# Optimization experiments

Hardware: AMD Instinct MI355X
Metric: run time of the kernel (lower is better)

## Reference

```python
import jax, jax.numpy as jnp
import numpy as np

H = 16   # heads
D = 64   # dim_heads
E = 1024 # embed_dim


def setup_inputs() -> dict:
    key = jax.random.key(0)
    ks = jax.random.split(key, 13)
    B, T = 4, 2048
    s_in = 1.0 / np.sqrt(E)
    s_out = 1.0 / np.sqrt(H * D)
    return {
        "q": jax.random.normal(ks[0], (B, T, E), jnp.float32),
        "k": jax.random.normal(ks[1], (B, T, E), jnp.float32),
        "v": jax.random.normal(ks[2], (B, T, E), jnp.float32),
        "Wq": jax.random.normal(ks[3], (E, H * D), jnp.float32) * s_in,
        "bq": jax.random.normal(ks[4], (H * D,), jnp.float32) * s_in,
        "Wk": jax.random.normal(ks[5], (E, H * D), jnp.float32) * s_in,
        "bk": jax.random.normal(ks[6], (H * D,), jnp.float32) * s_in,
        "Wv": jax.random.normal(ks[7], (E, H * D), jnp.float32) * s_in,
        "bv": jax.random.normal(ks[8], (H * D,), jnp.float32) * s_in,
        "Wo": jax.random.normal(ks[9], (H * D, E), jnp.float32) * s_out,
        "bo": jax.random.normal(ks[10], (E,), jnp.float32) * s_out,
    }


def reference(q, k, v, Wq, bq, Wk, bk, Wv, bv, Wo, bo):
    B, T, _ = q.shape
    scale = jnp.sqrt(jnp.asarray(E, q.dtype))  # note: sqrt(embed_dim), as in source
    # NOTE: source does .view(B, H, T, D) on contiguous (B, T, H*D) -> raw reshape.
    qh = (q @ Wq + bq).reshape(B, H, T, D)
    kh = (k @ Wk + bk).reshape(B, H, T, D)
    vh = (v @ Wv + bv).reshape(B, H, T, D)
    attn = jnp.einsum("bhtd,bhsd->bhts", qh, kh) / scale  # (B,H,T,T)
    causal = jnp.tril(jnp.ones((T, T), dtype=bool))
    attn = jnp.where(causal, attn, -jnp.inf)
    p = jax.nn.softmax(attn, axis=-1)
    out = jnp.einsum("bhts,bhsd->bhtd", p, vh)  # (B,H,T,D)
    out = out.transpose(0, 2, 1, 3).reshape(B, T, H * D)
    return out @ Wo + bo
```

## Files before the change

### kernel.cpp

```cpp
#include <hip/hip_runtime.h>
#include <hip/hip_bf16.h>
#include <math.h>


typedef unsigned short ushort_t;
typedef __attribute__((ext_vector_type(8))) short s8v;
typedef __attribute__((ext_vector_type(8))) unsigned short us8;
typedef __attribute__((ext_vector_type(4))) float f4v;

#define BAR()    __builtin_amdgcn_s_barrier()
#define LFENCE() asm volatile("" ::: "memory")
#define VMCNT(n) asm volatile("s_waitcnt vmcnt(" #n ")" ::: "memory")

__device__ __forceinline__ unsigned short f2bf(float x) {
  __hip_bfloat16 h = __float2bfloat16(x);
  unsigned short u; __builtin_memcpy(&u, &h, 2); return u;
}

__device__ __forceinline__ void gload16(const void* g, void* l) {
  __builtin_amdgcn_global_load_lds(
      (const __attribute__((address_space(1))) unsigned int*)g,
      (__attribute__((address_space(3))) unsigned int*)l, 16, 0, 0);
}

__global__ __launch_bounds__(256) void castk3(const float* __restrict__ q,
                                              const float* __restrict__ k,
                                              const float* __restrict__ v,
                                              ushort_t* __restrict__ dst) {
  const int y = blockIdx.y;
  const float* src = (y == 0) ? q : (y == 1) ? k : v;
  ushort_t* d = dst + (size_t)y * 8388608;
  int i = blockIdx.x * 256 + threadIdx.x;
  const float4* s4 = (const float4*)src + (size_t)i * 2;
  float4 a = s4[0], b = s4[1];
  us8 o;
  o[0]=f2bf(a.x); o[1]=f2bf(a.y); o[2]=f2bf(a.z); o[3]=f2bf(a.w);
  o[4]=f2bf(b.x); o[5]=f2bf(b.y); o[6]=f2bf(b.z); o[7]=f2bf(b.w);
  *(us8*)(d + (size_t)i * 8) = o;
}

__global__ __launch_bounds__(256) void wtrans4(
    const float* __restrict__ W0, const float* __restrict__ W1,
    const float* __restrict__ W2, const float* __restrict__ W3,
    ushort_t* __restrict__ Wt) {
  __shared__ unsigned tr[64][65];
  const int z = blockIdx.z;
  const float* W = (z == 0) ? W0 : (z == 1) ? W1 : (z == 2) ? W2 : W3;
  ushort_t* dst = Wt + (size_t)z * 1048576;
  const int k0 = blockIdx.y * 64, n0 = blockIdx.x * 64;
  const int tid = threadIdx.x;
  {
    const int rr = tid >> 4, c4 = tid & 15;
#pragma unroll
    for (int p = 0; p < 4; ++p) {
      const int k = p * 16 + rr;
      float4 v = *(const float4*)(W + (size_t)(k0 + k) * 1024 + n0 + c4 * 4);
      tr[c4*4+0][k] = f2bf(v.x); tr[c4*4+1][k] = f2bf(v.y);
      tr[c4*4+2][k] = f2bf(v.z); tr[c4*4+3][k] = f2bf(v.w);
    }
  }
  __syncthreads();
  const int r = tid >> 3, s = tid & 7;
#pragma unroll
  for (int p = 0; p < 2; ++p) {
    const int n = p * 32 + r;
    us8 o;
#pragma unroll
    for (int j = 0; j < 8; ++j) o[j] = (ushort_t)tr[n][s*8+j];
    *(us8*)(dst + (size_t)(n0 + n) * 1024 + k0 + s * 8) = o;
  }
}

__global__ __launch_bounds__(256) void vtrans(const ushort_t* __restrict__ Pv,
                                              ushort_t* __restrict__ Pvt) {
  __shared__ unsigned tr[64][65];
  const int t0 = blockIdx.x * 64, hd = blockIdx.y;
  const ushort_t* src = Pv + (size_t)hd * 131072;
  ushort_t* dst = Pvt + (size_t)hd * 131072;
  const int tid = threadIdx.x;
  const int r = tid >> 3, s = tid & 7;
#pragma unroll
  for (int p = 0; p < 2; ++p) {
    const int t = p * 32 + r;
    us8 v = *(const us8*)(src + (size_t)(t0 + t) * 64 + s * 8);
#pragma unroll
    for (int j = 0; j < 8; ++j) tr[s*8+j][t] = v[j];
  }
  __syncthreads();
#pragma unroll
  for (int p = 0; p < 2; ++p) {
    const int d = p * 32 + r;
    us8 o;
#pragma unroll
    for (int j = 0; j < 8; ++j) o[j] = (ushort_t)tr[d][s*8+j];
    *(us8*)(dst + (size_t)d * 2048 + t0 + s * 8) = o;
  }
}

template<int OUTF32>
__global__ __launch_bounds__(256) void gemm_bf16(
    const ushort_t* __restrict__ A, const ushort_t* __restrict__ Bt,
    const float* __restrict__ bias, void* __restrict__ Cout,
    int Mdim, int Ndim, int Kdim)
{
  __shared__ __align__(16) ushort_t As[2][128 * 64];
  __shared__ __align__(16) ushort_t Bs[2][128 * 64];
  const int tid = threadIdx.x;
  const int m0 = blockIdx.y * 128, n0 = blockIdx.x * 128;
  const int w = tid >> 6, lane = tid & 63, lo = lane & 15, hi = lane >> 4;
  const int wm = (w >> 1) * 64, wn = (w & 1) * 64;
  const int srow = tid >> 3, sslot = tid & 7;

  f4v acc[4][4];
#pragma unroll
  for (int i = 0; i < 4; ++i)
#pragma unroll
    for (int j = 0; j < 4; ++j) { f4v z = {0.f,0.f,0.f,0.f}; acc[i][j] = z; }

  const int NT = Kdim >> 6;

#define G_STAGE(buf, k0)                                                     \
  {                                                                          \
    _Pragma("unroll")                                                        \
    for (int i = 0; i < 4; ++i) {                                            \
      const int row = i * 32 + srow;                                         \
      const int sw = (sslot ^ (row & 7)) * 8;                                \
      gload16(A  + (size_t)(m0 + row) * Kdim + (k0) + sw,                    \
              &As[buf][(i * 256 + tid) * 8]);                                \
      gload16(Bt + (size_t)(n0 + row) * Kdim + (k0) + sw,                    \
              &Bs[buf][(i * 256 + tid) * 8]);                                \
    }                                                                        \
  }

  G_STAGE(0, 0);
  int cur = 0;
  for (int t = 0; t < NT; ++t) {
    if (t + 1 < NT) { G_STAGE(cur ^ 1, (t + 1) * 64); VMCNT(8); }
    else            { VMCNT(0); }
    BAR(); LFENCE();
    const ushort_t* Ab = &As[cur][0];
    const ushort_t* Bb = &Bs[cur][0];
#pragma unroll
    for (int ks = 0; ks < 2; ++ks) {
      const int slot = ks * 4 + hi;
      s8v av[4], bv[4];
#pragma unroll
      for (int i = 0; i < 4; ++i) {
        const int ra = wm + i * 16 + lo;
        av[i] = *(const s8v*)&Ab[ra * 64 + ((slot ^ (ra & 7)) << 3)];
        const int rb = wn + i * 16 + lo;
        bv[i] = *(const s8v*)&Bb[rb * 64 + ((slot ^ (rb & 7)) << 3)];
      }
#pragma unroll
      for (int am = 0; am < 4; ++am)
#pragma unroll
        for (int an = 0; an < 4; ++an)
          acc[am][an] = __builtin_amdgcn_mfma_f32_16x16x32_bf16(
              av[am], bv[an], acc[am][an], 0, 0, 0);
    }
    LFENCE(); BAR();
    cur ^= 1;
  }
#undef G_STAGE

#pragma unroll
  for (int an = 0; an < 4; ++an) {
    const int n = n0 + wn + an * 16 + lo;
    const float bsv = bias[n];
#pragma unroll
    for (int am = 0; am < 4; ++am) {
      const int mb = m0 + wm + am * 16 + hi * 4;
#pragma unroll
      for (int r = 0; r < 4; ++r) {
        const float v = acc[am][an][r] + bsv;
        if (OUTF32) ((float*)Cout)[(size_t)(mb + r) * Ndim + n] = v;
        else ((ushort_t*)Cout)[(size_t)(mb + r) * Ndim + n] = f2bf(v);
      }
    }
  }
}

__global__ __launch_bounds__(256) void attn_mfma(
    const ushort_t* __restrict__ Pq, const ushort_t* __restrict__ Pk,
    const ushort_t* __restrict__ Pvt, ushort_t* __restrict__ Ao)
{
  __shared__ __align__(16) ushort_t Ks[2][64 * 64];
  __shared__ __align__(16) ushort_t Vts[2][64 * 64];
  __shared__ __align__(16) ushort_t Psb[64 * 64];

  const int tid = threadIdx.x;
  const int id = blockIdx.x;
  const int qt = 31 - (id >> 6);
  const int hd = id & 63;
  const int b = hd >> 4, h = hd & 15;
  const int w = tid >> 6, lane = tid & 63, lo = lane & 15, hi = lane >> 4;
  const ushort_t* Qh = Pq + (size_t)hd * 131072;
  const ushort_t* Kh = Pk + (size_t)hd * 131072;
  const ushort_t* Vh = Pvt + (size_t)hd * 131072;
  const int srow = tid >> 3, sslot = tid & 7;

  s8v qa[2];
#pragma unroll
  for (int ks = 0; ks < 2; ++ks)
    qa[ks] = *(const s8v*)(Qh + (size_t)(qt * 64 + w * 16 + lo) * 64 + ks * 32 + hi * 8);

  f4v od[4];
#pragma unroll
  for (int f = 0; f < 4; ++f) { f4v z = {0.f,0.f,0.f,0.f}; od[f] = z; }
  float m[4], l[4];
#pragma unroll
  for (int r = 0; r < 4; ++r) { m[r] = -INFINITY; l[r] = 0.f; }

#define A_STAGE(buf, kt_)                                                    \
  {                                                                          \
    _Pragma("unroll")                                                        \
    for (int i = 0; i < 2; ++i) {                                            \
      const int row = i * 32 + srow;                                         \
      const int sw = (sslot ^ (row & 7)) * 8;                                \
      gload16(Kh + (size_t)((kt_) * 64 + row) * 64 + sw,                     \
              &Ks[buf][(i * 256 + tid) * 8]);                                \
      gload16(Vh + (size_t)row * 2048 + (kt_) * 64 + sw,                     \
              &Vts[buf][(i * 256 + tid) * 8]);                               \
    }                                                                        \
  }

  A_STAGE(0, 0);
  int cur = 0;
  for (int kt = 0; kt <= qt; ++kt) {
    if (kt < qt) { A_STAGE(cur ^ 1, kt + 1); VMCNT(4); }
    else         { VMCNT(0); }
    BAR(); LFENCE();
    const ushort_t* Kb = &Ks[cur][0];
    const ushort_t* Vb = &Vts[cur][0];

    f4v sf[4];
#pragma unroll
    for (int f = 0; f < 4; ++f) { f4v z = {0.f,0.f,0.f,0.f}; sf[f] = z; }
    __builtin_amdgcn_s_setprio(1);
#pragma unroll
    for (int ks = 0; ks < 2; ++ks) {
      const int slot = ks * 4 + hi;
      s8v kb[4];
#pragma unroll
      for (int f = 0; f < 4; ++f) {
        const int rk = f * 16 + lo;
        kb[f] = *(const s8v*)&Kb[rk * 64 + ((slot ^ (rk & 7)) << 3)];
      }
#pragma unroll
      for (int f = 0; f < 4; ++f)
        sf[f] = __builtin_amdgcn_mfma_f32_16x16x32_bf16(qa[ks], kb[f], sf[f], 0, 0, 0);
    }
    __builtin_amdgcn_s_setprio(0);

    float sc[4][4];
#pragma unroll
    for (int f = 0; f < 4; ++f)
#pragma unroll
      for (int r = 0; r < 4; ++r) sc[r][f] = sf[f][r] * 0.03125f;
    if (kt == qt) {
#pragma unroll
      for (int r = 0; r < 4; ++r)
#pragma unroll
        for (int f = 0; f < 4; ++f)
          if (16 * f + lo > 16 * w + 4 * hi + r) sc[r][f] = -INFINITY;
    }
    float rmax[4];
#pragma unroll
    for (int r = 0; r < 4; ++r)
      rmax[r] = fmaxf(fmaxf(sc[r][0], sc[r][1]), fmaxf(sc[r][2], sc[r][3]));
#pragma unroll
    for (int x = 1; x < 16; x <<= 1)
#pragma unroll
      for (int r = 0; r < 4; ++r) rmax[r] = fmaxf(rmax[r], __shfl_xor(rmax[r], x, 64));
#pragma unroll
    for (int r = 0; r < 4; ++r) {
      const float mn = fmaxf(m[r], rmax[r]);
      const float al = __expf(m[r] - mn);
      m[r] = mn;
      float rs = 0.f;
#pragma unroll
      for (int f = 0; f < 4; ++f) {
        const float p = __expf(sc[r][f] - mn);
        sc[r][f] = p; rs += p;
      }
      l[r] = l[r] * al + rs;
#pragma unroll
      for (int f = 0; f < 4; ++f) od[f][r] *= al;
    }

#pragma unroll
    for (int r = 0; r < 4; ++r) {
      const int t = 16 * w + 4 * hi + r;
#pragma unroll
      for (int f = 0; f < 4; ++f) {
        const int s = 16 * f + lo;
        Psb[t * 64 + (((s >> 3) ^ (t & 7)) << 3) + (s & 7)] = f2bf(sc[r][f]);
      }
    }

    {
      const int t = 16 * w + lo;
      __builtin_amdgcn_s_setprio(1);
#pragma unroll
      for (int ks = 0; ks < 2; ++ks) {
        const int slot = ks * 4 + hi;
        s8v pa = *(const s8v*)&Psb[t * 64 + ((slot ^ (t & 7)) << 3)];
        s8v vb[4];
#pragma unroll
        for (int f = 0; f < 4; ++f) {
          const int rd = f * 16 + lo;
          vb[f] = *(const s8v*)&Vb[rd * 64 + ((slot ^ (rd & 7)) << 3)];
        }
#pragma unroll
        for (int f = 0; f < 4; ++f)
          od[f] = __builtin_amdgcn_mfma_f32_16x16x32_bf16(pa, vb[f], od[f], 0, 0, 0);
      }
      __builtin_amdgcn_s_setprio(0);
    }
    LFENCE(); BAR();
    cur ^= 1;
  }
#undef A_STAGE

#pragma unroll
  for (int x = 1; x < 16; x <<= 1)
#pragma unroll
    for (int r = 0; r < 4; ++r) l[r] += __shfl_xor(l[r], x, 64);
  float inv[4];
#pragma unroll
  for (int r = 0; r < 4; ++r) inv[r] = 1.0f / l[r];
#pragma unroll
  for (int f = 0; f < 4; ++f)
#pragma unroll
    for (int r = 0; r < 4; ++r) {
      const int t = qt * 64 + 16 * w + 4 * hi + r;
      const int d = 16 * f + lo;
      Ao[(size_t)(b * 2048 + t) * 1024 + h * 64 + d] = f2bf(od[f][r] * inv[r]);
    }
}

extern "C" void kernel_launch(void* const* d_in, const int* in_sizes, int n_in,
                              void* d_out, int out_size, void* d_ws, size_t ws_size,
                              hipStream_t stream) {
  const float* q  = (const float*)d_in[0];
  const float* k  = (const float*)d_in[1];
  const float* v  = (const float*)d_in[2];
  const float* Wq = (const float*)d_in[3];
  const float* bq = (const float*)d_in[4];
  const float* Wk = (const float*)d_in[5];
  const float* bk = (const float*)d_in[6];
  const float* Wv = (const float*)d_in[7];
  const float* bv = (const float*)d_in[8];
  const float* Wo = (const float*)d_in[9];
  const float* bo = (const float*)d_in[10];
  float* out = (float*)d_out;

  char* wsb = (char*)d_ws;
  ushort_t* qb  = (ushort_t*)(wsb + 0);
  ushort_t* kb  = (ushort_t*)(wsb + 16777216);
  ushort_t* Wqt = (ushort_t*)(wsb + 50331648);
  ushort_t* Pq  = (ushort_t*)(wsb + 58720256);
  ushort_t* Pk  = (ushort_t*)(wsb + 75497472);
  ushort_t* Pv  = (ushort_t*)(wsb + 92274688);
  ushort_t* Wkt = Wqt + 1048576;
  ushort_t* Wvt = Wqt + 2097152;
  ushort_t* Wot = Wqt + 3145728;
  ushort_t* vb  = (ushort_t*)(wsb + 33554432);
  ushort_t* Pvt = qb;
  ushort_t* Ao  = kb;

  castk3<<<dim3(4096, 3), 256, 0, stream>>>(q, k, v, qb);
  wtrans4<<<dim3(16, 16, 4), 256, 0, stream>>>(Wq, Wk, Wv, Wo, Wqt);

  gemm_bf16<0><<<dim3(8, 64), 256, 0, stream>>>(qb, Wqt, bq, Pq, 8192, 1024, 1024);
  gemm_bf16<0><<<dim3(8, 64), 256, 0, stream>>>(kb, Wkt, bk, Pk, 8192, 1024, 1024);
  gemm_bf16<0><<<dim3(8, 64), 256, 0, stream>>>(vb, Wvt, bv, Pv, 8192, 1024, 1024);

  vtrans<<<dim3(32, 64), 256, 0, stream>>>(Pv, Pvt);
  attn_mfma<<<2048, 256, 0, stream>>>(Pq, Pk, Pvt, Ao);

  gemm_bf16<1><<<dim3(8, 64), 256, 0, stream>>>(Ao, Wot, bo, out, 8192, 1024, 1024);
}
```

Measured before the change: 367.9 us.

## Batch QKV GEMMs, enlarge attention tiles, fold scale into Q, use exp2 with lazy rescale

Merges the three projection GEMMs into one launch with a z-dimension and bakes log2e/sqrt(E) into the Q projection output. The attention kernel now uses 512 threads covering 128 query rows per block, and uses exp2 instead of exp. It skips the cross-lane max reduction and rescale when no row max grows by more than a threshold. The K loop is unrolled by two with fixed buffers, and the GEMM dimensions are hardcoded. This cuts launch count, repeated K/V loads and softmax overhead, at the cost of extra masking work on the diagonal and a larger block.

```diff
diff --git a/kernel.cpp b/kernel.cpp
--- a/kernel.cpp
+++ b/kernel.cpp
@@ -15,6 +15,10 @@
 __device__ __forceinline__ unsigned short f2bf(float x) {
   __hip_bfloat16 h = __float2bfloat16(x);
   unsigned short u; __builtin_memcpy(&u, &h, 2); return u;
+}
+
+__device__ __forceinline__ float exp2a(float x) {
+  return __builtin_amdgcn_exp2f(x);
 }
 
 __device__ __forceinline__ void gload16(const void* g, void* l) {
@@ -98,15 +102,13 @@
 }
 
 template<int OUTF32>
-__global__ __launch_bounds__(256) void gemm_bf16(
+__device__ __forceinline__ void gemm_body(
+    ushort_t* As, ushort_t* Bs,
     const ushort_t* __restrict__ A, const ushort_t* __restrict__ Bt,
     const float* __restrict__ bias, void* __restrict__ Cout,
-    int Mdim, int Ndim, int Kdim)
+    float scale, int m0, int n0)
 {
-  __shared__ __align__(16) ushort_t As[2][128 * 64];
-  __shared__ __align__(16) ushort_t Bs[2][128 * 64];
   const int tid = threadIdx.x;
-  const int m0 = blockIdx.y * 128, n0 = blockIdx.x * 128;
   const int w = tid >> 6, lane = tid & 63, lo = lane & 15, hi = lane >> 4;
   const int wm = (w >> 1) * 64, wn = (w & 1) * 64;
   const int srow = tid >> 3, sslot = tid & 7;
@@ -117,29 +119,19 @@
 #pragma unroll
     for (int j = 0; j < 4; ++j) { f4v z = {0.f,0.f,0.f,0.f}; acc[i][j] = z; }
 
-  const int NT = Kdim >> 6;
-
-#define G_STAGE(buf, k0)                                                     \
-  {                                                                          \
-    _Pragma("unroll")                                                        \
-    for (int i = 0; i < 4; ++i) {                                            \
-      const int row = i * 32 + srow;                                         \
-      const int sw = (sslot ^ (row & 7)) * 8;                                \
-      gload16(A  + (size_t)(m0 + row) * Kdim + (k0) + sw,                    \
-              &As[buf][(i * 256 + tid) * 8]);                                \
-      gload16(Bt + (size_t)(n0 + row) * Kdim + (k0) + sw,                    \
-              &Bs[buf][(i * 256 + tid) * 8]);                                \
-    }                                                                        \
-  }
-
-  G_STAGE(0, 0);
-  int cur = 0;
-  for (int t = 0; t < NT; ++t) {
-    if (t + 1 < NT) { G_STAGE(cur ^ 1, (t + 1) * 64); VMCNT(8); }
-    else            { VMCNT(0); }
-    BAR(); LFENCE();
-    const ushort_t* Ab = &As[cur][0];
-    const ushort_t* Bb = &Bs[cur][0];
+  auto stage = [&](int buf, int kt) {
+    ushort_t* Ad = &As[buf * 8192];
+    ushort_t* Bd = &Bs[buf * 8192];
+#pragma unroll
+    for (int i = 0; i < 4; ++i) {
+      const int row = i * 32 + srow;
+      const int sw = (sslot ^ (row & 7)) * 8;
+      gload16(A  + (size_t)(m0 + row) * 1024 + kt * 64 + sw, &Ad[(i * 256 + tid) * 8]);
+      gload16(Bt + (size_t)(n0 + row) * 1024 + kt * 64 + sw, &Bd[(i * 256 + tid) * 8]);
+    }
+  };
+
+  auto compute = [&](const ushort_t* Ab, const ushort_t* Bb) {
 #pragma unroll
     for (int ks = 0; ks < 2; ++ks) {
       const int slot = ks * 4 + hi;
@@ -158,10 +150,20 @@
           acc[am][an] = __builtin_amdgcn_mfma_f32_16x16x32_bf16(
               av[am], bv[an], acc[am][an], 0, 0, 0);
     }
+  };
+
+  stage(0, 0);
+  for (int t = 0; t < 16; t += 2) {
+    stage(1, t + 1); VMCNT(8);
+    BAR(); LFENCE();
+    compute(&As[0], &Bs[0]);
     LFENCE(); BAR();
-    cur ^= 1;
-  }
-#undef G_STAGE
+    if (t + 2 < 16) { stage(0, t + 2); VMCNT(8); }
+    else            { VMCNT(0); }
+    BAR(); LFENCE();
+    compute(&As[8192], &Bs[8192]);
+    LFENCE(); BAR();
+  }
 
 #pragma unroll
   for (int an = 0; an < 4; ++an) {
@@ -172,25 +174,51 @@
       const int mb = m0 + wm + am * 16 + hi * 4;
 #pragma unroll
       for (int r = 0; r < 4; ++r) {
-        const float v = acc[am][an][r] + bsv;
-        if (OUTF32) ((float*)Cout)[(size_t)(mb + r) * Ndim + n] = v;
-        else ((ushort_t*)Cout)[(size_t)(mb + r) * Ndim + n] = f2bf(v);
-      }
-    }
-  }
-}
-
-__global__ __launch_bounds__(256) void attn_mfma(
+        const float v = (acc[am][an][r] + bsv) * scale;
+        if (OUTF32) ((float*)Cout)[(size_t)(mb + r) * 1024 + n] = v;
+        else ((ushort_t*)Cout)[(size_t)(mb + r) * 1024 + n] = f2bf(v);
+      }
+    }
+  }
+}
+
+__global__ __launch_bounds__(256) void gemm_qkv(
+    const ushort_t* __restrict__ Abase, const ushort_t* __restrict__ Wbase,
+    const float* __restrict__ bq, const float* __restrict__ bk,
+    const float* __restrict__ bv, ushort_t* __restrict__ Cbase)
+{
+  __shared__ __align__(16) ushort_t As[2 * 8192];
+  __shared__ __align__(16) ushort_t Bs[2 * 8192];
+  const int z = blockIdx.z;
+  const ushort_t* A  = Abase + (size_t)z * 8388608;
+  const ushort_t* Bt = Wbase + (size_t)z * 1048576;
+  const float* bias = (z == 0) ? bq : (z == 1) ? bk : bv;
+  const float scale = (z == 0) ? 0.04508422002778011f : 1.0f;
+  gemm_body<0>(As, Bs, A, Bt, bias, Cbase + (size_t)z * 8388608,
+               scale, blockIdx.y * 128, blockIdx.x * 128);
+}
+
+__global__ __launch_bounds__(256) void gemm_out(
+    const ushort_t* __restrict__ A, const ushort_t* __restrict__ Bt,
+    const float* __restrict__ bias, float* __restrict__ Cout)
+{
+  __shared__ __align__(16) ushort_t As[2 * 8192];
+  __shared__ __align__(16) ushort_t Bs[2 * 8192];
+  gemm_body<1>(As, Bs, A, Bt, bias, Cout, 1.0f,
+               blockIdx.y * 128, blockIdx.x * 128);
+}
+
+__global__ __launch_bounds__(512) void attn_mfma(
     const ushort_t* __restrict__ Pq, const ushort_t* __restrict__ Pk,
     const ushort_t* __restrict__ Pvt, ushort_t* __restrict__ Ao)
 {
-  __shared__ __align__(16) ushort_t Ks[2][64 * 64];
-  __shared__ __align__(16) ushort_t Vts[2][64 * 64];
-  __shared__ __align__(16) ushort_t Psb[64 * 64];
+  __shared__ __align__(16) ushort_t Ks[2 * 4096];
+  __shared__ __align__(16) ushort_t Vts[2 * 4096];
+  __shared__ __align__(16) ushort_t Psb[128 * 64];
 
   const int tid = threadIdx.x;
   const int id = blockIdx.x;
-  const int qt = 31 - (id >> 6);
+  const int qt = 15 - (id >> 6);
   const int hd = id & 63;
   const int b = hd >> 4, h = hd & 15;
   const int w = tid >> 6, lane = tid & 63, lo = lane & 15, hi = lane >> 4;
@@ -198,41 +226,31 @@
   const ushort_t* Kh = Pk + (size_t)hd * 131072;
   const ushort_t* Vh = Pvt + (size_t)hd * 131072;
   const int srow = tid >> 3, sslot = tid & 7;
+  const int qt2 = 2 * qt;
 
   s8v qa[2];
 #pragma unroll
   for (int ks = 0; ks < 2; ++ks)
-    qa[ks] = *(const s8v*)(Qh + (size_t)(qt * 64 + w * 16 + lo) * 64 + ks * 32 + hi * 8);
+    qa[ks] = *(const s8v*)(Qh + (size_t)(qt * 128 + w * 16 + lo) * 64 + ks * 32 + hi * 8);
 
   f4v od[4];
 #pragma unroll
   for (int f = 0; f < 4; ++f) { f4v z = {0.f,0.f,0.f,0.f}; od[f] = z; }
   float m[4], l[4];
-#pragma unroll
-  for (int r = 0; r < 4; ++r) { m[r] = -INFINITY; l[r] = 0.f; }
-
-#define A_STAGE(buf, kt_)                                                    \
-  {                                                                          \
-    _Pragma("unroll")                                                        \
-    for (int i = 0; i < 2; ++i) {                                            \
-      const int row = i * 32 + srow;                                         \
-      const int sw = (sslot ^ (row & 7)) * 8;                                \
-      gload16(Kh + (size_t)((kt_) * 64 + row) * 64 + sw,                     \
-              &Ks[buf][(i * 256 + tid) * 8]);                                \
-      gload16(Vh + (size_t)row * 2048 + (kt_) * 64 + sw,                     \
-              &Vts[buf][(i * 256 + tid) * 8]);                               \
-    }                                                                        \
-  }
-
-  A_STAGE(0, 0);
-  int cur = 0;
-  for (int kt = 0; kt <= qt; ++kt) {
-    if (kt < qt) { A_STAGE(cur ^ 1, kt + 1); VMCNT(4); }
-    else         { VMCNT(0); }
-    BAR(); LFENCE();
-    const ushort_t* Kb = &Ks[cur][0];
-    const ushort_t* Vb = &Vts[cur][0];
-
+  int tg[4];
+#pragma unroll
+  for (int r = 0; r < 4; ++r) {
+    m[r] = -INFINITY; l[r] = 0.f;
+    tg[r] = qt * 128 + 16 * w + 4 * hi + r;
+  }
+
+  auto astage = [&](int buf, int kt) {
+    const int sw = (sslot ^ (srow & 7)) * 8;
+    gload16(Kh + (size_t)(kt * 64 + srow) * 64 + sw, &Ks[buf * 4096 + tid * 8]);
+    gload16(Vh + (size_t)srow * 2048 + kt * 64 + sw, &Vts[buf * 4096 + tid * 8]);
+  };
+
+  auto acompute = [&](const ushort_t* Kb, const ushort_t* Vb, int kt_) {
     f4v sf[4];
 #pragma unroll
     for (int f = 0; f < 4; ++f) { f4v z = {0.f,0.f,0.f,0.f}; sf[f] = z; }
@@ -256,36 +274,48 @@
 #pragma unroll
     for (int f = 0; f < 4; ++f)
 #pragma unroll
-      for (int r = 0; r < 4; ++r) sc[r][f] = sf[f][r] * 0.03125f;
-    if (kt == qt) {
+      for (int r = 0; r < 4; ++r) sc[r][f] = sf[f][r];
+    if (kt_ >= qt2) {
 #pragma unroll
       for (int r = 0; r < 4; ++r)
 #pragma unroll
         for (int f = 0; f < 4; ++f)
-          if (16 * f + lo > 16 * w + 4 * hi + r) sc[r][f] = -INFINITY;
-    }
-    float rmax[4];
+          if (kt_ * 64 + 16 * f + lo > tg[r]) sc[r][f] = -INFINITY;
+    }
+
+    float lmax[4];
 #pragma unroll
     for (int r = 0; r < 4; ++r)
-      rmax[r] = fmaxf(fmaxf(sc[r][0], sc[r][1]), fmaxf(sc[r][2], sc[r][3]));
-#pragma unroll
-    for (int x = 1; x < 16; x <<= 1)
-#pragma unroll
-      for (int r = 0; r < 4; ++r) rmax[r] = fmaxf(rmax[r], __shfl_xor(rmax[r], x, 64));
+      lmax[r] = fmaxf(fmaxf(sc[r][0], sc[r][1]), fmaxf(sc[r][2], sc[r][3]));
+    const int ok = (lmax[0] <= m[0] + 8.f) & (lmax[1] <= m[1] + 8.f) &
+                   (lmax[2] <= m[2] + 8.f) & (lmax[3] <= m[3] + 8.f);
+    if (!__all(ok)) {
+      float rmax[4];
+#pragma unroll
+      for (int r = 0; r < 4; ++r) rmax[r] = lmax[r];
+#pragma unroll
+      for (int x = 1; x < 16; x <<= 1)
+#pragma unroll
+        for (int r = 0; r < 4; ++r)
+          rmax[r] = fmaxf(rmax[r], __shfl_xor(rmax[r], x, 64));
+#pragma unroll
+      for (int r = 0; r < 4; ++r) {
+        const float mn = fmaxf(m[r], rmax[r]);
+        const float al = exp2a(m[r] - mn);
+        m[r] = mn; l[r] *= al;
+#pragma unroll
+        for (int f = 0; f < 4; ++f) od[f][r] *= al;
+      }
+    }
 #pragma unroll
     for (int r = 0; r < 4; ++r) {
-      const float mn = fmaxf(m[r], rmax[r]);
-      const float al = __expf(m[r] - mn);
-      m[r] = mn;
       float rs = 0.f;
 #pragma unroll
       for (int f = 0; f < 4; ++f) {
-        const float p = __expf(sc[r][f] - mn);
+        const float p = exp2a(sc[r][f] - m[r]);
         sc[r][f] = p; rs += p;
       }
-      l[r] = l[r] * al + rs;
-#pragma unroll
-      for (int f = 0; f < 4; ++f) od[f][r] *= al;
+      l[r] += rs;
     }
 
 #pragma unroll
@@ -317,10 +347,21 @@
       }
       __builtin_amdgcn_s_setprio(0);
     }
+  };
+
+  const int NT = qt2 + 2;
+  astage(0, 0);
+  for (int t2 = 0; t2 < NT; t2 += 2) {
+    astage(1, t2 + 1); VMCNT(2);
+    BAR(); LFENCE();
+    acompute(&Ks[0], &Vts[0], t2);
     LFENCE(); BAR();
-    cur ^= 1;
-  }
-#undef A_STAGE
+    if (t2 + 2 < NT) { astage(0, t2 + 2); VMCNT(2); }
+    else             { VMCNT(0); }
+    BAR(); LFENCE();
+    acompute(&Ks[4096], &Vts[4096], t2 + 1);
+    LFENCE(); BAR();
+  }
 
 #pragma unroll
   for (int x = 1; x < 16; x <<= 1)
@@ -333,9 +374,8 @@
   for (int f = 0; f < 4; ++f)
 #pragma unroll
     for (int r = 0; r < 4; ++r) {
-      const int t = qt * 64 + 16 * w + 4 * hi + r;
       const int d = 16 * f + lo;
-      Ao[(size_t)(b * 2048 + t) * 1024 + h * 64 + d] = f2bf(od[f][r] * inv[r]);
+      Ao[(size_t)(b * 2048 + tg[r]) * 1024 + h * 64 + d] = f2bf(od[f][r] * inv[r]);
     }
 }
 
@@ -357,27 +397,21 @@
 
   char* wsb = (char*)d_ws;
   ushort_t* qb  = (ushort_t*)(wsb + 0);
-  ushort_t* kb  = (ushort_t*)(wsb + 16777216);
   ushort_t* Wqt = (ushort_t*)(wsb + 50331648);
   ushort_t* Pq  = (ushort_t*)(wsb + 58720256);
-  ushort_t* Pk  = (ushort_t*)(wsb + 75497472);
+  ushort_t* kbb = (ushort_t*)(wsb + 16777216);
   ushort_t* Pv  = (ushort_t*)(wsb + 92274688);
-  ushort_t* Wkt = Wqt + 1048576;
-  ushort_t* Wvt = Wqt + 2097152;
   ushort_t* Wot = Wqt + 3145728;
-  ushort_t* vb  = (ushort_t*)(wsb + 33554432);
   ushort_t* Pvt = qb;
-  ushort_t* Ao  = kb;
+  ushort_t* Ao  = kbb;
 
   castk3<<<dim3(4096, 3), 256, 0, stream>>>(q, k, v, qb);
   wtrans4<<<dim3(16, 16, 4), 256, 0, stream>>>(Wq, Wk, Wv, Wo, Wqt);
 
-  gemm_bf16<0><<<dim3(8, 64), 256, 0, stream>>>(qb, Wqt, bq, Pq, 8192, 1024, 1024);
-  gemm_bf16<0><<<dim3(8, 64), 256, 0, stream>>>(kb, Wkt, bk, Pk, 8192, 1024, 1024);
-  gemm_bf16<0><<<dim3(8, 64), 256, 0, stream>>>(vb, Wvt, bv, Pv, 8192, 1024, 1024);
+  gemm_qkv<<<dim3(8, 64, 3), 256, 0, stream>>>(qb, Wqt, bq, bk, bv, Pq);
 
   vtrans<<<dim3(32, 64), 256, 0, stream>>>(Pv, Pvt);
-  attn_mfma<<<2048, 256, 0, stream>>>(Pq, Pk, Pvt, Ao);
-
-  gemm_bf16<1><<<dim3(8, 64), 256, 0, stream>>>(Ao, Wot, bo, out, 8192, 1024, 1024);
-}
+  attn_mfma<<<1024, 512, 0, stream>>>(Pq, Pq + 8388608, Pvt, Ao);
+
+  gemm_out<<<dim3(8, 64), 256, 0, stream>>>(Ao, Wot, bo, out);
+}
```

Measured after the change: 337.3 us. 8.3% less time.
